# Performance work log

Measured on AMD Instinct MI355X. Metric: run time of the kernel, lower is better.

## Reference

```python
import jax, jax.numpy as jnp
import numpy as np

D_NODE = 128
D_EDGE = 128
D_HID = 128
D_OUT = 128
N_NODES = 50000
N_EDGES = 500000
LN_EPS = 1e-5


def setup_inputs() -> dict:
    key = jax.random.key(0)
    ks = jax.random.split(key, 10)
    d_cat = 2 * D_NODE + D_EDGE  # 384
    inv = lambda d: 1.0 / np.sqrt(d)
    return {
        "efeat": jax.random.normal(ks[0], (N_EDGES, D_EDGE), jnp.float32),
        "nfeat": jax.random.normal(ks[1], (N_NODES, D_NODE), jnp.float32),
        "src": jax.random.randint(ks[2], (N_EDGES,), 0, N_NODES),
        "dst": jax.random.randint(ks[3], (N_EDGES,), 0, N_NODES),
        # MLP params: Linear(d_cat, hid) -> SiLU -> Linear(hid, out) -> LayerNorm(out)
        "W1": jax.random.uniform(ks[4], (d_cat, D_HID), jnp.float32, -inv(d_cat), inv(d_cat)),
        "b1": jnp.zeros((D_HID,), jnp.float32),
        "W2": jax.random.uniform(ks[5], (D_HID, D_OUT), jnp.float32, -inv(D_HID), inv(D_HID)),
        "b2": jnp.zeros((D_OUT,), jnp.float32),
        "gamma": jnp.ones((D_OUT,), jnp.float32),
        "beta": jnp.zeros((D_OUT,), jnp.float32),
    }


def _layernorm(x, gamma, beta):
    mu = jnp.mean(x, axis=-1, keepdims=True)
    var = jnp.mean(jnp.square(x - mu), axis=-1, keepdims=True)
    return (x - mu) * jax.lax.rsqrt(var + LN_EPS) * gamma + beta


def reference(efeat, nfeat, src, dst, W1, b1, W2, b2, gamma, beta):
    # gather source/target node feats per edge and concat with edge feats: [E, 2*Dn+De]
    cat_feat = jnp.concatenate([efeat, nfeat[src], nfeat[dst]], axis=-1)
    h = jax.nn.silu(cat_feat @ W1 + b1)          # [E, hid]
    out = _layernorm(h @ W2 + b2, gamma, beta)    # [E, out]
    efeat_new = out + efeat                        # residual
    return (efeat_new, nfeat)
```

## Files before the change

### kernel.cpp

```cpp
#include <hip/hip_runtime.h>
#include <hip/hip_bf16.h>

#define N_EDGES 500000
#define N_NODES 50000
#define NT ((N_EDGES + 63) / 64)
#define GRID 256
#define LN_EPS 1e-5f

typedef __attribute__((ext_vector_type(8))) short bf16x8;
typedef __attribute__((ext_vector_type(4))) short bf16x4;
typedef __attribute__((ext_vector_type(4))) float f32x4;

static __device__ __forceinline__ short f2bf(float f) {
  return __builtin_bit_cast(short, __float2bfloat16(f));
}
static __device__ __forceinline__ float bf2f(short s) {
  unsigned u = ((unsigned)(unsigned short)s) << 16;
  return __builtin_bit_cast(float, u);
}
static __device__ __forceinline__ void gload16(const void* g, void* l) {
  __builtin_amdgcn_global_load_lds(
      (const __attribute__((address_space(1))) unsigned int*)g,
      (__attribute__((address_space(3))) unsigned int*)l, 16, 0, 0);
}
static __device__ __forceinline__ void bar_lds() {
  __builtin_amdgcn_sched_barrier(0);
  asm volatile("s_waitcnt lgkmcnt(0)" ::: "memory");
  __builtin_amdgcn_s_barrier();
  __builtin_amdgcn_sched_barrier(0);
}
static __device__ __forceinline__ void bar_vm8() {
  __builtin_amdgcn_sched_barrier(0);
  asm volatile("s_waitcnt vmcnt(8) lgkmcnt(0)" ::: "memory");
  __builtin_amdgcn_s_barrier();
  __builtin_amdgcn_sched_barrier(0);
}

__global__ void convert_kernel(const float* __restrict__ W1,
                               const float* __restrict__ W2,
                               const float* __restrict__ nfeat,
                               short* __restrict__ w1t, short* __restrict__ w2t,
                               short* __restrict__ nbf, float* __restrict__ outn) {
  const int step = gridDim.x * blockDim.x;
  const int t0 = blockIdx.x * blockDim.x + threadIdx.x;
  for (int i = t0; i < 384 * 128; i += step) {
    int n = i / 384, k = i - n * 384;
    w1t[i] = f2bf(W1[k * 128 + n]);
  }
  for (int i = t0; i < 128 * 128; i += step) {
    int n = i >> 7, k = i & 127;
    w2t[i] = f2bf(W2[k * 128 + n]);
  }
  for (int i = t0; i < N_NODES * 128 / 4; i += step) {
    f32x4 v = *(const f32x4*)(nfeat + (size_t)i * 4);
    short o4[4];
#pragma unroll
    for (int q = 0; q < 4; ++q) o4[q] = f2bf(v[q]);
    *(unsigned long long*)(nbf + (size_t)i * 4) = *(unsigned long long*)o4;
    *(f32x4*)(outn + (size_t)i * 4) = v;
  }
}

__global__ __launch_bounds__(512, 2) void edge_mlp_pipelined(
    const float* __restrict__ efeat, const short* __restrict__ nbf,
    const int* __restrict__ src, const int* __restrict__ dst,
    const short* __restrict__ w1t, const short* __restrict__ w2t,
    const float* __restrict__ b1, const float* __restrict__ b2,
    const float* __restrict__ gamma, const float* __restrict__ beta,
    float* __restrict__ out) {
  __shared__ __align__(16) char smem[132096];
  char* Hb = smem + 98304;
  char* xb = smem + 114688;
  float* gb = (float*)(smem + 131072);

  const int tid = threadIdx.x;
  const int lane = tid & 63;
  const int w = tid >> 6;
  const int wm = w >> 2;
  const int wn = w & 3;
  const int lrow = lane & 15;
  const int kgrp = (lane >> 4) & 3;
  if (tid < 256) gb[tid] = tid < 128 ? gamma[tid] : beta[tid - 128];

  bf16x8 B1[12][2], B2[4][2];
  float b1v[2], b2v[2];
#pragma unroll
  for (int n = 0; n < 2; ++n) {
    const int c = wn * 32 + n * 16 + lrow;
    b1v[n] = b1[c];
    b2v[n] = b2[c];
#pragma unroll
    for (int ks = 0; ks < 12; ++ks)
      B1[ks][n] = *(const bf16x8*)(w1t + c * 384 + ks * 32 + kgrp * 8);
#pragma unroll
    for (int ks = 0; ks < 4; ++ks)
      B2[ks][n] = *(const bf16x8*)(w2t + c * 128 + ks * 32 + kgrp * 8);
  }

  int grow[4], goff[4], gseg[4];
#pragma unroll
  for (int i = 0; i < 4; ++i) {
    int F = w * 4096 + i * 1024 + lane * 16;
    grow[i] = F >> 9;
    int win = F & 511;
    gseg[i] = win >> 8;
    goff[i] = (win & 255) ^ ((grow[i] & 15) << 4);
  }
  const int frow = tid >> 3;
  const int fcb = tid & 7;
  const int fswz = (frow & 15) << 4;

  f32x4 S[4];
  auto stage_S = [&](int t) {
    int e = t * 64 + frow;
    e = e < N_EDGES ? e : (N_EDGES - 1);
#pragma unroll
    for (int it = 0; it < 4; ++it)
      S[it] = *(const f32x4*)(efeat + (size_t)e * 128 + (fcb + it * 8) * 4);
  };
  auto write_ef = [&](char* buf) {
#pragma unroll
    for (int it = 0; it < 4; ++it) {
      bf16x4 v;
#pragma unroll
      for (int j = 0; j < 4; ++j) v[j] = f2bf(S[it][j]);
      *(bf16x4*)(buf + frow * 256 + (((fcb + it * 8) * 8) ^ fswz)) = v;
    }
  };
  int idxN[4];
  auto load_idx = [&](int t, int* ix) {
#pragma unroll
    for (int i = 0; i < 4; ++i) {
      int e = t * 64 + grow[i];
      e = e < N_EDGES ? e : (N_EDGES - 1);
      ix[i] = gseg[i] ? dst[e] : src[e];
    }
  };
  auto issue_g = [&](char* buf, const int* ix) {
#pragma unroll
    for (int i = 0; i < 4; ++i)
      gload16((const char*)nbf + (size_t)ix[i] * 256 + goff[i],
              buf + 16384 + w * 4096 + i * 1024);
  };

  const int t0 = blockIdx.x;
  char* cur = smem;
  char* nxt = smem + 49152;
  {
    int ix0[4];
    load_idx(t0, ix0);
    stage_S(t0);
    write_ef(cur);
    issue_g(cur, ix0);
    load_idx(t0 + GRID, idxN);
  }

  for (int t = t0; t < NT; t += GRID) {
    stage_S(t + GRID);
    issue_g(nxt, idxN);
    bar_vm8();
    load_idx(t + 2 * GRID, idxN);

    f32x4 acc[2][2];
#pragma unroll
    for (int m = 0; m < 2; ++m)
#pragma unroll
      for (int n = 0; n < 2; ++n) acc[m][n] = (f32x4)0.f;
#pragma unroll
    for (int ks = 0; ks < 12; ++ks) {
      bf16x8 a[2];
#pragma unroll
      for (int m = 0; m < 2; ++m) {
        int row = wm * 32 + m * 16 + lrow;
        int sw = (row & 15) << 4;
        a[m] = (ks < 4)
                   ? *(const bf16x8*)(cur + row * 256 + ((ks * 64 + kgrp * 16) ^ sw))
                   : *(const bf16x8*)(cur + 16384 + row * 512 +
                                      (((ks - 4) * 64 + kgrp * 16) ^ sw));
      }
#pragma unroll
      for (int m = 0; m < 2; ++m)
#pragma unroll
        for (int n = 0; n < 2; ++n)
          acc[m][n] = __builtin_amdgcn_mfma_f32_16x16x32_bf16(a[m], B1[ks][n],
                                                              acc[m][n], 0, 0, 0);
    }

#pragma unroll
    for (int m = 0; m < 2; ++m)
#pragma unroll
      for (int n = 0; n < 2; ++n)
#pragma unroll
        for (int r = 0; r < 4; ++r) {
          float x = acc[m][n][r] + b1v[n];
          float h = x / (1.f + __expf(-x));
          int row = wm * 32 + m * 16 + kgrp * 4 + r;
          int col = wn * 32 + n * 16 + lrow;
          *(short*)(Hb + row * 256 + ((col * 2) ^ ((row & 15) << 4))) = f2bf(h);
        }
    bar_lds();

    f32x4 acc2[2][2];
#pragma unroll
    for (int m = 0; m < 2; ++m)
#pragma unroll
      for (int n = 0; n < 2; ++n) acc2[m][n] = (f32x4)0.f;
#pragma unroll
    for (int ks = 0; ks < 4; ++ks) {
      bf16x8 a[2];
#pragma unroll
      for (int m = 0; m < 2; ++m) {
        int row = wm * 32 + m * 16 + lrow;
        a[m] = *(const bf16x8*)(Hb + row * 256 +
                                ((ks * 64 + kgrp * 16) ^ ((row & 15) << 4)));
      }
#pragma unroll
      for (int m = 0; m < 2; ++m)
#pragma unroll
        for (int n = 0; n < 2; ++n)
          acc2[m][n] = __builtin_amdgcn_mfma_f32_16x16x32_bf16(a[m], B2[ks][n],
                                                               acc2[m][n], 0, 0, 0);
    }

#pragma unroll
    for (int m = 0; m < 2; ++m)
#pragma unroll
      for (int n = 0; n < 2; ++n)
#pragma unroll
        for (int r = 0; r < 4; ++r) {
          float x = acc2[m][n][r] + b2v[n];
          int row = wm * 32 + m * 16 + kgrp * 4 + r;
          int col = wn * 32 + n * 16 + lrow;
          *(short*)(xb + row * 256 + ((col * 2) ^ ((row & 15) << 4))) = f2bf(x);
        }
    bar_lds();

    {
      bf16x4 xv[4];
      float s1 = 0.f, s2 = 0.f;
#pragma unroll
      for (int it = 0; it < 4; ++it) {
        int c4 = fcb + it * 8;
        xv[it] = *(const bf16x4*)(xb + frow * 256 + ((c4 * 8) ^ fswz));
#pragma unroll
        for (int j = 0; j < 4; ++j) {
          float f = bf2f(xv[it][j]);
          s1 += f;
          s2 += f * f;
        }
      }
      s1 += __shfl_xor(s1, 1, 64); s2 += __shfl_xor(s2, 1, 64);
      s1 += __shfl_xor(s1, 2, 64); s2 += __shfl_xor(s2, 2, 64);
      s1 += __shfl_xor(s1, 4, 64); s2 += __shfl_xor(s2, 4, 64);
      float mu = s1 * (1.f / 128.f);
      float var = s2 * (1.f / 128.f) - mu * mu;
      float rs = rsqrtf(var + LN_EPS);
      int e = t * 64 + frow;
      if (e < N_EDGES) {
        float* op = out + (size_t)e * 128;
#pragma unroll
        for (int it = 0; it < 4; ++it) {
          int c4 = fcb + it * 8;
          bf16x4 rv = *(const bf16x4*)(cur + frow * 256 + ((c4 * 8) ^ fswz));
          f32x4 g = *(const f32x4*)(gb + c4 * 4);
          f32x4 be = *(const f32x4*)(gb + 128 + c4 * 4);
          f32x4 o;
#pragma unroll
          for (int j = 0; j < 4; ++j)
            o[j] = (bf2f(xv[it][j]) - mu) * rs * g[j] + be[j] + bf2f(rv[j]);
          *(f32x4*)(op + c4 * 4) = o;
        }
      }
    }
    write_ef(nxt);
    char* tmp = cur; cur = nxt; nxt = tmp;
  }
  asm volatile("s_waitcnt vmcnt(0)" ::: "memory");
}

__global__ void edge_simple(const float* __restrict__ efeat, const float* __restrict__ nfeat,
                            const int* __restrict__ src, const int* __restrict__ dst,
                            const float* __restrict__ W1, const float* __restrict__ b1,
                            const float* __restrict__ W2, const float* __restrict__ b2,
                            const float* __restrict__ g, const float* __restrict__ be,
                            float* __restrict__ out) {
  int e = blockIdx.x, j = threadIdx.x;
  __shared__ float cat[384], h[128], red[128];
  cat[j] = efeat[(size_t)e * 128 + j];
  cat[128 + j] = nfeat[(size_t)src[e] * 128 + j];
  cat[256 + j] = nfeat[(size_t)dst[e] * 128 + j];
  __syncthreads();
  float s = b1[j];
  for (int k = 0; k < 384; ++k) s += cat[k] * W1[k * 128 + j];
  h[j] = s / (1.f + expf(-s));
  __syncthreads();
  float o = b2[j];
  for (int k = 0; k < 128; ++k) o += h[k] * W2[k * 128 + j];
  red[j] = o;
  __syncthreads();
  __shared__ float mu, rs;
  if (j == 0) {
    float s1 = 0, s2 = 0;
    for (int k = 0; k < 128; ++k) { s1 += red[k]; s2 += red[k] * red[k]; }
    mu = s1 / 128.f;
    rs = rsqrtf(s2 / 128.f - mu * mu + LN_EPS);
  }
  __syncthreads();
  out[(size_t)e * 128 + j] = (o - mu) * rs * g[j] + be[j] + efeat[(size_t)e * 128 + j];
}

extern "C" void kernel_launch(void* const* d_in, const int* in_sizes, int n_in,
                              void* d_out, int out_size, void* d_ws, size_t ws_size,
                              hipStream_t stream) {
  const float* efeat = (const float*)d_in[0];
  const float* nfeat = (const float*)d_in[1];
  const int* src = (const int*)d_in[2];
  const int* dst = (const int*)d_in[3];
  const float* W1 = (const float*)d_in[4];
  const float* b1 = (const float*)d_in[5];
  const float* W2 = (const float*)d_in[6];
  const float* b2 = (const float*)d_in[7];
  const float* gamma = (const float*)d_in[8];
  const float* beta = (const float*)d_in[9];
  float* out = (float*)d_out;

  short* w1t = (short*)d_ws;
  short* w2t = w1t + 384 * 128;
  short* nbf = w2t + 128 * 128;
  const size_t need =
      (size_t)(384 * 128 + 128 * 128 + (size_t)N_NODES * 128) * sizeof(short);

  if (ws_size >= need) {
    convert_kernel<<<1024, 256, 0, stream>>>(W1, W2, nfeat, w1t, w2t, nbf,
                                             out + (size_t)N_EDGES * 128);
    edge_mlp_pipelined<<<GRID, 512, 0, stream>>>(efeat, nbf, src, dst, w1t, w2t,
                                                 b1, b2, gamma, beta, out);
  } else {
    hipMemcpyAsync(out + (size_t)N_EDGES * 128, nfeat,
                   (size_t)N_NODES * 128 * sizeof(float),
                   hipMemcpyDeviceToDevice, stream);
    edge_simple<<<N_EDGES, 128, 0, stream>>>(efeat, nfeat, src, dst, W1, b1, W2,
                                             b2, gamma, beta, out);
  }
}
```

Before: 333.4 us.

## Shrink LDS and drop register-resident weights to run four blocks per CU

Shared memory drops from about 129 KB to 80 KB by using one efeat tile buffer and reusing the gather buffer for the hidden and LN scratch. W1/W2 fragments are no longer kept in registers and are instead reloaded from global memory (through cache) on every k-step. Gamma and beta are also read from global memory. Launch bounds move to 4 blocks per CU and GRID to 512. The gather prefetch is now issued after the first GEMM and the vmcnt-bounded barrier is removed. This trades repeated weight loads and a less overlapped gather pipeline for higher occupancy, and it depends on the new __syncthreads and lgkmcnt barriers to order the gather loads correctly.

```diff
diff --git a/kernel.cpp b/kernel.cpp
--- a/kernel.cpp
+++ b/kernel.cpp
@@ -4,7 +4,7 @@
 #define N_EDGES 500000
 #define N_NODES 50000
 #define NT ((N_EDGES + 63) / 64)
-#define GRID 256
+#define GRID 512
 #define LN_EPS 1e-5f
 
 typedef __attribute__((ext_vector_type(8))) short bf16x8;
@@ -26,12 +26,6 @@
 static __device__ __forceinline__ void bar_lds() {
   __builtin_amdgcn_sched_barrier(0);
   asm volatile("s_waitcnt lgkmcnt(0)" ::: "memory");
-  __builtin_amdgcn_s_barrier();
-  __builtin_amdgcn_sched_barrier(0);
-}
-static __device__ __forceinline__ void bar_vm8() {
-  __builtin_amdgcn_sched_barrier(0);
-  asm volatile("s_waitcnt vmcnt(8) lgkmcnt(0)" ::: "memory");
   __builtin_amdgcn_s_barrier();
   __builtin_amdgcn_sched_barrier(0);
 }
@@ -61,17 +55,15 @@
   }
 }
 
-__global__ __launch_bounds__(512, 2) void edge_mlp_pipelined(
+__global__ __launch_bounds__(512, 4) void edge_mlp_pipelined(
     const float* __restrict__ efeat, const short* __restrict__ nbf,
     const int* __restrict__ src, const int* __restrict__ dst,
     const short* __restrict__ w1t, const short* __restrict__ w2t,
     const float* __restrict__ b1, const float* __restrict__ b2,
     const float* __restrict__ gamma, const float* __restrict__ beta,
     float* __restrict__ out) {
-  __shared__ __align__(16) char smem[132096];
-  char* Hb = smem + 98304;
-  char* xb = smem + 114688;
-  float* gb = (float*)(smem + 131072);
+  __shared__ __align__(16) char smem[81920];
+  char* efb = smem;
 
   const int tid = threadIdx.x;
   const int lane = tid & 63;
@@ -80,21 +72,11 @@
   const int wn = w & 3;
   const int lrow = lane & 15;
   const int kgrp = (lane >> 4) & 3;
-  if (tid < 256) gb[tid] = tid < 128 ? gamma[tid] : beta[tid - 128];
-
-  bf16x8 B1[12][2], B2[4][2];
   float b1v[2], b2v[2];
 #pragma unroll
   for (int n = 0; n < 2; ++n) {
-    const int c = wn * 32 + n * 16 + lrow;
-    b1v[n] = b1[c];
-    b2v[n] = b2[c];
-#pragma unroll
-    for (int ks = 0; ks < 12; ++ks)
-      B1[ks][n] = *(const bf16x8*)(w1t + c * 384 + ks * 32 + kgrp * 8);
-#pragma unroll
-    for (int ks = 0; ks < 4; ++ks)
-      B2[ks][n] = *(const bf16x8*)(w2t + c * 128 + ks * 32 + kgrp * 8);
+    b1v[n] = b1[wn * 32 + n * 16 + lrow];
+    b2v[n] = b2[wn * 32 + n * 16 + lrow];
   }
 
   int grow[4], goff[4], gseg[4];
@@ -118,13 +100,13 @@
     for (int it = 0; it < 4; ++it)
       S[it] = *(const f32x4*)(efeat + (size_t)e * 128 + (fcb + it * 8) * 4);
   };
-  auto write_ef = [&](char* buf) {
+  auto write_ef = [&]() {
 #pragma unroll
     for (int it = 0; it < 4; ++it) {
       bf16x4 v;
 #pragma unroll
       for (int j = 0; j < 4; ++j) v[j] = f2bf(S[it][j]);
-      *(bf16x4*)(buf + frow * 256 + (((fcb + it * 8) * 8) ^ fswz)) = v;
+      *(bf16x4*)(efb + frow * 256 + (((fcb + it * 8) * 8) ^ fswz)) = v;
     }
   };
   int idxN[4];
@@ -140,26 +122,30 @@
 #pragma unroll
     for (int i = 0; i < 4; ++i)
       gload16((const char*)nbf + (size_t)ix[i] * 256 + goff[i],
-              buf + 16384 + w * 4096 + i * 1024);
+              buf + w * 4096 + i * 1024);
   };
 
   const int t0 = blockIdx.x;
-  char* cur = smem;
+  char* cur = smem + 16384;
   char* nxt = smem + 49152;
   {
+    stage_S(t0);
+    write_ef();
     int ix0[4];
     load_idx(t0, ix0);
-    stage_S(t0);
-    write_ef(cur);
     issue_g(cur, ix0);
     load_idx(t0 + GRID, idxN);
   }
 
   for (int t = t0; t < NT; t += GRID) {
+    __syncthreads();
+
+    bf16x4 rz[4];
+#pragma unroll
+    for (int it = 0; it < 4; ++it)
+      rz[it] = *(const bf16x4*)(efb + frow * 256 + (((fcb + it * 8) * 8) ^ fswz));
+
     stage_S(t + GRID);
-    issue_g(nxt, idxN);
-    bar_vm8();
-    load_idx(t + 2 * GRID, idxN);
 
     f32x4 acc[2][2];
 #pragma unroll
@@ -168,23 +154,34 @@
       for (int n = 0; n < 2; ++n) acc[m][n] = (f32x4)0.f;
 #pragma unroll
     for (int ks = 0; ks < 12; ++ks) {
+      bf16x8 B1f[2];
+#pragma unroll
+      for (int n = 0; n < 2; ++n)
+        B1f[n] = *(const bf16x8*)(w1t + (wn * 32 + n * 16 + lrow) * 384 +
+                                  ks * 32 + kgrp * 8);
       bf16x8 a[2];
 #pragma unroll
       for (int m = 0; m < 2; ++m) {
         int row = wm * 32 + m * 16 + lrow;
         int sw = (row & 15) << 4;
         a[m] = (ks < 4)
-                   ? *(const bf16x8*)(cur + row * 256 + ((ks * 64 + kgrp * 16) ^ sw))
-                   : *(const bf16x8*)(cur + 16384 + row * 512 +
+                   ? *(const bf16x8*)(efb + row * 256 + ((ks * 64 + kgrp * 16) ^ sw))
+                   : *(const bf16x8*)(cur + row * 512 +
                                       (((ks - 4) * 64 + kgrp * 16) ^ sw));
       }
 #pragma unroll
       for (int m = 0; m < 2; ++m)
 #pragma unroll
         for (int n = 0; n < 2; ++n)
-          acc[m][n] = __builtin_amdgcn_mfma_f32_16x16x32_bf16(a[m], B1[ks][n],
+          acc[m][n] = __builtin_amdgcn_mfma_f32_16x16x32_bf16(a[m], B1f[n],
                                                               acc[m][n], 0, 0, 0);
     }
+
+    issue_g(nxt, idxN);
+    load_idx(t + 2 * GRID, idxN);
+
+    bar_lds();
+    write_ef();
 
 #pragma unroll
     for (int m = 0; m < 2; ++m)
@@ -196,7 +193,7 @@
           float h = x / (1.f + __expf(-x));
           int row = wm * 32 + m * 16 + kgrp * 4 + r;
           int col = wn * 32 + n * 16 + lrow;
-          *(short*)(Hb + row * 256 + ((col * 2) ^ ((row & 15) << 4))) = f2bf(h);
+          *(short*)(cur + row * 256 + ((col * 2) ^ ((row & 15) << 4))) = f2bf(h);
         }
     bar_lds();
 
@@ -207,18 +204,23 @@
       for (int n = 0; n < 2; ++n) acc2[m][n] = (f32x4)0.f;
 #pragma unroll
     for (int ks = 0; ks < 4; ++ks) {
+      bf16x8 B2f[2];
+#pragma unroll
+      for (int n = 0; n < 2; ++n)
+        B2f[n] = *(const bf16x8*)(w2t + (wn * 32 + n * 16 + lrow) * 128 +
+                                  ks * 32 + kgrp * 8);
       bf16x8 a[2];
 #pragma unroll
       for (int m = 0; m < 2; ++m) {
         int row = wm * 32 + m * 16 + lrow;
-        a[m] = *(const bf16x8*)(Hb + row * 256 +
+        a[m] = *(const bf16x8*)(cur + row * 256 +
                                 ((ks * 64 + kgrp * 16) ^ ((row & 15) << 4)));
       }
 #pragma unroll
       for (int m = 0; m < 2; ++m)
 #pragma unroll
         for (int n = 0; n < 2; ++n)
-          acc2[m][n] = __builtin_amdgcn_mfma_f32_16x16x32_bf16(a[m], B2[ks][n],
+          acc2[m][n] = __builtin_amdgcn_mfma_f32_16x16x32_bf16(a[m], B2f[n],
                                                                acc2[m][n], 0, 0, 0);
     }
 
@@ -231,7 +233,8 @@
           float x = acc2[m][n][r] + b2v[n];
           int row = wm * 32 + m * 16 + kgrp * 4 + r;
           int col = wn * 32 + n * 16 + lrow;
-          *(short*)(xb + row * 256 + ((col * 2) ^ ((row & 15) << 4))) = f2bf(x);
+          *(short*)(cur + 16384 + row * 256 + ((col * 2) ^ ((row & 15) << 4))) =
+              f2bf(x);
         }
     bar_lds();
 
@@ -241,7 +244,7 @@
 #pragma unroll
       for (int it = 0; it < 4; ++it) {
         int c4 = fcb + it * 8;
-        xv[it] = *(const bf16x4*)(xb + frow * 256 + ((c4 * 8) ^ fswz));
+        xv[it] = *(const bf16x4*)(cur + 16384 + frow * 256 + ((c4 * 8) ^ fswz));
 #pragma unroll
         for (int j = 0; j < 4; ++j) {
           float f = bf2f(xv[it][j]);
@@ -261,18 +264,16 @@
 #pragma unroll
         for (int it = 0; it < 4; ++it) {
           int c4 = fcb + it * 8;
-          bf16x4 rv = *(const bf16x4*)(cur + frow * 256 + ((c4 * 8) ^ fswz));
-          f32x4 g = *(const f32x4*)(gb + c4 * 4);
-          f32x4 be = *(const f32x4*)(gb + 128 + c4 * 4);
+          f32x4 g = *(const f32x4*)(gamma + c4 * 4);
+          f32x4 be = *(const f32x4*)(beta + c4 * 4);
           f32x4 o;
 #pragma unroll
           for (int j = 0; j < 4; ++j)
-            o[j] = (bf2f(xv[it][j]) - mu) * rs * g[j] + be[j] + bf2f(rv[j]);
+            o[j] = (bf2f(xv[it][j]) - mu) * rs * g[j] + be[j] + bf2f(rz[it][j]);
           *(f32x4*)(op + c4 * 4) = o;
         }
       }
     }
-    write_ef(nxt);
     char* tmp = cur; cur = nxt; nxt = tmp;
   }
   asm volatile("s_waitcnt vmcnt(0)" ::: "memory");
```

After: 417.8 us. 25.3% more time.
